# Optimization experiments

Hardware: AMD Instinct MI355X
Metric: run time of the kernel (lower is better)

Reference implementation:

```python
import jax, jax.numpy as jnp
import numpy as np

B, TV, TE = 128, 32, 64
VOCAB, EMB, H, REPR, NET, MAXLEN = 1024, 256, 512, 128, 8, 32


def setup_inputs() -> dict:
    key = jax.random.key(0)
    ks = jax.random.split(key, 26)
    g = lambda i, shape: jax.random.normal(ks[i], shape, dtype=jnp.float32) * 0.05
    return dict(
        input_vertex=jax.random.randint(ks[0], (B, TV), 0, VOCAB),
        input_edge=jax.random.randint(ks[1], (B, TE, 3), 0, NET),
        vertex_emb=g(2, (VOCAB, EMB)),
        v_Wi=g(3, (3 * H, EMB)), v_Wh=g(4, (3 * H, H)), v_bi=g(5, (3 * H,)), v_bh=g(6, (3 * H,)),
        vout_W=g(7, (VOCAB, H)), vout_b=g(8, (VOCAB,)),
        vrep_W=g(9, (REPR, H)), vrep_b=g(10, (REPR,)),
        edge_emb=g(11, (MAXLEN, EMB)),
        e_Wi=g(12, (3 * H, 2 * EMB)), e_Wh=g(13, (3 * H, H)), e_bi=g(14, (3 * H,)), e_bh=g(15, (3 * H,)),
        erep_W=g(16, (REPR, H)), erep_b=g(17, (REPR,)),
        etype_W=g(18, (NET, REPR)), etype_b=g(19, (NET,)),
        src_w=g(20, (REPR,)), src_b=g(21, ()),
        dst_w=g(22, (REPR,)), dst_b=g(23, ()),
    )


def _gru_scan(X, Wi, Wh, bi, bh):
    # X: [T, B, D] -> hidden states [T, B, H]; torch GRUCell gate order r,z,n
    gi = jnp.einsum('tbd,gd->tbg', X, Wi) + bi  # precompute input projections
    h0 = jnp.zeros((X.shape[1], Wh.shape[1]), X.dtype)

    def step(h, gi_t):
        gh = h @ Wh.T + bh
        ir, iz, inn = jnp.split(gi_t, 3, axis=-1)
        hr, hz, hn = jnp.split(gh, 3, axis=-1)
        r = jax.nn.sigmoid(ir + hr)
        z = jax.nn.sigmoid(iz + hz)
        n = jnp.tanh(inn + r * hn)
        h_new = (1.0 - z) * n + z * h
        return h_new, h_new

    _, hs = jax.lax.scan(step, h0, gi)
    return hs


def reference(input_vertex, input_edge, vertex_emb, v_Wi, v_Wh, v_bi, v_bh,
              vout_W, vout_b, vrep_W, vrep_b, edge_emb, e_Wi, e_Wh, e_bi, e_bh,
              erep_W, erep_b, etype_W, etype_b, src_w, src_b, dst_w, dst_b):
    # ---- vertex RNN ----
    Ve = vertex_emb[input_vertex].transpose(1, 0, 2)          # [Tv, B, emb]
    hv = _gru_scan(Ve, v_Wi, v_Wh, v_bi, v_bh)                # [Tv, B, H]
    O_vertex = jnp.einsum('tbh,vh->bvt', hv, vout_W) + vout_b[None, :, None]  # [B, vocab, Tv]
    vrep = jnp.einsum('tbh,rh->tbr', hv, vrep_W) + vrep_b     # [Tv, B, repr]

    # ---- edge RNN ----
    E = jnp.concatenate([edge_emb[input_edge[:, :, 0]],
                         edge_emb[input_edge[:, :, 1]]], axis=2)  # [B, Te, 2*emb]
    he = _gru_scan(E.transpose(1, 0, 2), e_Wi, e_Wh, e_bi, e_bh)  # [Te, B, H]
    e = jnp.einsum('tbh,rh->tbr', he, erep_W) + erep_b            # [Te, B, repr]
    O_edge_type = jnp.einsum('ebr,kr->bke', e, etype_W) + etype_b[None, :, None]  # [B, n_et, Te]

    # ---- edge-vertex additive attention: tanh(e + v) ----
    u = jnp.tanh(e[:, None] + vrep[None])                     # [Te, Tv, B, repr]
    osrc = jnp.einsum('evbr,r->bve', u, src_w) + src_b        # [B, Tv, Te]
    odst = jnp.einsum('evbr,r->bve', u, dst_w) + dst_b        # [B, Tv, Te]
    O_edge = jnp.stack([osrc, odst], axis=2)                  # [B, Tv, 2, Te]

    return O_vertex, O_edge, O_edge_type
```

## Files before the change

### kernel.cpp

```cpp
#include <hip/hip_runtime.h>
#include <hip/hip_bf16.h>


typedef __bf16 bf16_t;
typedef bf16_t bf16x8 __attribute__((ext_vector_type(8)));
typedef bf16_t bf16x4 __attribute__((ext_vector_type(4)));
typedef float  f32x4  __attribute__((ext_vector_type(4)));
typedef unsigned long long ull_t;

#define OFF_GIV  0ull
#define OFF_GIE  6291456ull
#define OFF_HV   18874368ull
#define OFF_HE   20971520ull
#define OFF_VREP 25165824ull
#define OFF_EREP 25690112ull
#define OFF_HBUF 26738688ull
#define FLAG_BYTE_OFF  54001664ull
#define GICNT_BYTE_OFF 54002176ull
#define OFF_CVT  27002880ull
#define CVT_VEMB  0ull
#define CVT_EEMB  262144ull
#define CVT_VWI   270336ull
#define CVT_EWI   663552ull
#define CVT_VWH   1449984ull
#define CVT_EWH   2236416ull
#define CVT_VOUT  3022848ull
#define CVT_VREPW 3547136ull
#define CVT_EREPW 3612672ull

#define OUT_OV 0ull
#define OUT_OE 4194304ull
#define OUT_OT 4718592ull

__device__ __forceinline__ float fsigmoid(float x) {
    float e = __builtin_amdgcn_exp2f(-x * 1.4426950408889634f);
    return __builtin_amdgcn_rcpf(1.0f + e);
}
__device__ __forceinline__ float ftanh(float x) {
    x = fminf(x, 15.0f);
    float e = __builtin_amdgcn_exp2f(x * 2.8853900817779268f);
    return (e - 1.0f) * __builtin_amdgcn_rcpf(e + 1.0f);
}

__global__ __launch_bounds__(256) void prep_kernel(
    const float* __restrict__ vemb, const float* __restrict__ eemb,
    const float* __restrict__ vwi,  const float* __restrict__ ewi,
    const float* __restrict__ vwh,  const float* __restrict__ ewh,
    const float* __restrict__ voutw, const float* __restrict__ vrepw,
    const float* __restrict__ erepw, bf16_t* __restrict__ cvt,
    int* __restrict__ gicnt)
{
    int blk = blockIdx.x;
    if (blk >= 3592) {
        if (threadIdx.x < 128) gicnt[threadIdx.x] = 0;
        return;
    }
    const float* src; bf16_t* dst; int lb;
    if (blk < 256)       { src = vemb;  dst = cvt + CVT_VEMB;  lb = blk; }
    else if (blk < 264)  { src = eemb;  dst = cvt + CVT_EEMB;  lb = blk - 256; }
    else if (blk < 648)  { src = vwi;   dst = cvt + CVT_VWI;   lb = blk - 264; }
    else if (blk < 1416) { src = ewi;   dst = cvt + CVT_EWI;   lb = blk - 648; }
    else if (blk < 2184) { src = vwh;   dst = cvt + CVT_VWH;   lb = blk - 1416; }
    else if (blk < 2952) { src = ewh;   dst = cvt + CVT_EWH;   lb = blk - 2184; }
    else if (blk < 3464) { src = voutw; dst = cvt + CVT_VOUT;  lb = blk - 2952; }
    else if (blk < 3528) { src = vrepw; dst = cvt + CVT_VREPW; lb = blk - 3464; }
    else                 { src = erepw; dst = cvt + CVT_EREPW; lb = blk - 3528; }
    int idx = lb * 1024 + threadIdx.x * 4;
    float4 v = *(const float4*)(src + idx);
    bf16x4 o;
    o[0] = (bf16_t)v.x; o[1] = (bf16_t)v.y; o[2] = (bf16_t)v.z; o[3] = (bf16_t)v.w;
    *(bf16x4*)(dst + idx) = o;
}

template<int GATHER, int K>
__device__ __forceinline__ void produce_gi(
    const bf16_t* __restrict__ W, const float* __restrict__ bias,
    bf16_t* __restrict__ C, const int* __restrict__ gidx,
    const bf16_t* __restrict__ emb, int* __restrict__ cnt, int bx, int nbase)
{
    constexpr int K32 = K / 32;
    const int tid = threadIdx.x, lane = tid & 63, wv = tid >> 6;
    const int r16 = lane & 15, quad = lane >> 4, koff = quad * 8;
    const int mbase = bx * 512 + wv * 64;

    const bf16_t* ap0[4];
    const bf16_t* ap1[4];
#pragma unroll
    for (int i = 0; i < 4; ++i) {
        int row = mbase + i * 16 + r16;
        int b = row & 127, t = row >> 7;
        if (GATHER == 1) {
            ap0[i] = emb + (size_t)gidx[b * 32 + t] * 256 + koff;
            ap1[i] = ap0[i];
        } else {
            int c = (b * 64 + t) * 3;
            ap0[i] = emb + (size_t)gidx[c] * 256 + koff;
            ap1[i] = emb + (size_t)gidx[c + 1] * 256 + koff;
        }
    }
    const bf16_t* bp[4];
#pragma unroll
    for (int j = 0; j < 4; ++j)
        bp[j] = W + (size_t)(nbase + j * 16 + r16) * K + koff;

    f32x4 acc[4][4];
#pragma unroll
    for (int i = 0; i < 4; ++i)
#pragma unroll
        for (int j = 0; j < 4; ++j) acc[i][j] = (f32x4){0.f, 0.f, 0.f, 0.f};

    for (int kc = 0; kc < K32; ++kc) {
        bf16x8 a[4], b[4];
#pragma unroll
        for (int i = 0; i < 4; ++i) {
            const bf16_t* p;
            if (GATHER == 2) p = (kc < 8) ? (ap0[i] + kc * 32) : (ap1[i] + (kc - 8) * 32);
            else             p = ap0[i] + kc * 32;
            a[i] = *(const bf16x8*)p;
        }
#pragma unroll
        for (int j = 0; j < 4; ++j) b[j] = *(const bf16x8*)(bp[j] + kc * 32);
#pragma unroll
        for (int i = 0; i < 4; ++i)
#pragma unroll
            for (int j = 0; j < 4; ++j)
                acc[i][j] = __builtin_amdgcn_mfma_f32_16x16x32_bf16(a[i], b[j], acc[i][j], 0, 0, 0);
    }

#pragma unroll
    for (int j = 0; j < 4; ++j) {
        int col = nbase + j * 16 + r16;
        float bf = bias[col];
#pragma unroll
        for (int i = 0; i < 4; ++i) {
#pragma unroll
            for (int q = 0; q < 4; ++q) {
                int row = mbase + i * 16 + quad * 4 + q;
                bf16_t hb = (bf16_t)(acc[i][j][q] + bf);
                __hip_atomic_store((unsigned short*)(C + (size_t)row * 1536 + col),
                                   __builtin_bit_cast(unsigned short, hb),
                                   __ATOMIC_RELAXED, __HIP_MEMORY_SCOPE_AGENT);
            }
        }
    }
    __builtin_amdgcn_s_waitcnt(0);
    __syncthreads();
    if (tid < 4)
        __hip_atomic_fetch_add(&cnt[bx * 4 + tid], 1,
                               __ATOMIC_RELAXED, __HIP_MEMORY_SCOPE_AGENT);
}

template<int OUTMODE, int K>
__device__ __forceinline__ void consume_gemm(
    const bf16_t* __restrict__ A, const bf16_t* __restrict__ W,
    const float* __restrict__ bias, void* __restrict__ Cv,
    int N, int bx, int nbase)
{
    constexpr int K32 = K / 32;
    const int tid = threadIdx.x, lane = tid & 63, wv = tid >> 6;
    const int r16 = lane & 15, quad = lane >> 4, koff = quad * 8;
    const int mbase = bx * 512 + wv * 64;

    const bf16_t* ap[4];
#pragma unroll
    for (int i = 0; i < 4; ++i)
        ap[i] = A + (size_t)(mbase + i * 16 + r16) * K + koff;
    const bf16_t* bp[4];
#pragma unroll
    for (int j = 0; j < 4; ++j)
        bp[j] = W + (size_t)(nbase + j * 16 + r16) * K + koff;

    f32x4 acc[4][4];
#pragma unroll
    for (int i = 0; i < 4; ++i)
#pragma unroll
        for (int j = 0; j < 4; ++j) acc[i][j] = (f32x4){0.f, 0.f, 0.f, 0.f};

    for (int kc = 0; kc < K32; ++kc) {
        bf16x8 a[4], b[4];
#pragma unroll
        for (int i = 0; i < 4; ++i) a[i] = *(const bf16x8*)(ap[i] + kc * 32);
#pragma unroll
        for (int j = 0; j < 4; ++j) b[j] = *(const bf16x8*)(bp[j] + kc * 32);
#pragma unroll
        for (int i = 0; i < 4; ++i)
#pragma unroll
            for (int j = 0; j < 4; ++j)
                acc[i][j] = __builtin_amdgcn_mfma_f32_16x16x32_bf16(a[i], b[j], acc[i][j], 0, 0, 0);
    }

#pragma unroll
    for (int j = 0; j < 4; ++j) {
        int col = nbase + j * 16 + r16;
        float bf = bias[col];
#pragma unroll
        for (int i = 0; i < 4; ++i) {
            int rowq = mbase + i * 16 + quad * 4;
            if (OUTMODE == 1) {
                int b = rowq >> 5, t0 = rowq & 31;
                float4 v4;
                v4.x = acc[i][j][0] + bf; v4.y = acc[i][j][1] + bf;
                v4.z = acc[i][j][2] + bf; v4.w = acc[i][j][3] + bf;
                *(float4*)((float*)Cv + ((size_t)(b * 1024) + col) * 32 + t0) = v4;
            } else {
                bf16_t* C = (bf16_t*)Cv;
#pragma unroll
                for (int q = 0; q < 4; ++q) {
                    bf16_t hb = (bf16_t)(acc[i][j][q] + bf);
                    __hip_atomic_store(
                        (unsigned short*)(C + (size_t)(rowq + q) * N + col),
                        __builtin_bit_cast(unsigned short, hb),
                        __ATOMIC_RELAXED, __HIP_MEMORY_SCOPE_AGENT);
                }
            }
        }
    }
}

__device__ __forceinline__ void gate_on(int* p, int thresh) {
    if (threadIdx.x == 0) {
        while (__hip_atomic_load(p, __ATOMIC_RELAXED,
                                 __HIP_MEMORY_SCOPE_AGENT) < thresh)
            __builtin_amdgcn_s_sleep(8);
    }
    __syncthreads();
    asm volatile("" ::: "memory");
}

__global__ __launch_bounds__(512) void fused_scan(
    bf16_t* __restrict__ giV, bf16_t* __restrict__ giE,
    const bf16_t* __restrict__ WhV, const bf16_t* __restrict__ WhE,
    const float* __restrict__ bhV, const float* __restrict__ bhE,
    bf16_t* __restrict__ hV, bf16_t* __restrict__ hE,
    bf16_t* __restrict__ hbuf, int* __restrict__ flags, int* __restrict__ gicnt,
    const int* __restrict__ ivtx, const int* __restrict__ iedg,
    const bf16_t* __restrict__ vemb, const bf16_t* __restrict__ eemb,
    const bf16_t* __restrict__ vwi, const bf16_t* __restrict__ ewi,
    const float* __restrict__ vbi, const float* __restrict__ ebi,
    const bf16_t* __restrict__ voutw, const float* __restrict__ voutb,
    const bf16_t* __restrict__ vrepw, const float* __restrict__ vrepb,
    const bf16_t* __restrict__ erepw, const float* __restrict__ erepb,
    bf16_t* __restrict__ vrep, bf16_t* __restrict__ erep,
    const float* __restrict__ etypeW, const float* __restrict__ etypeB,
    const float* __restrict__ src_w, const float* __restrict__ src_b,
    const float* __restrict__ dst_w, const float* __restrict__ dst_b,
    float* __restrict__ out)
{
    __shared__ __align__(16) char lds_all[83968];
    bf16_t (*hbf)[520] = (bf16_t (*)[520])lds_all;
    f32x4 (*red)[3][64] = (f32x4 (*)[3][64])(lds_all + 33280);

    const int bid = blockIdx.x;

    if (bid >= 128) {
        const int tid = threadIdx.x;
        if (bid < 512) {
            int g3 = bid - 128;
            int bx = g3 / 24, nb = g3 - bx * 24;
            produce_gi<2, 512>(ewi, ebi, giE, iedg, eemb, gicnt + 32, bx, nb * 64);
        } else if (bid < 704) {
            int g2 = bid - 512;
            int bx = g2 / 24, nb = g2 - bx * 24;
            produce_gi<1, 256>(vwi, vbi, giV, ivtx, vemb, gicnt, bx, nb * 64);
        } else if (bid < 832) {
            gate_on(&gicnt[96], 64);
            int cb = bid - 704;
            consume_gemm<1, 512>(hV, voutw, voutb, out, 1024, cb & 7, (cb >> 3) * 64);
        } else if (bid < 848) {
            gate_on(&gicnt[96], 64);
            int cb = bid - 832;
            consume_gemm<0, 512>(hV, vrepw, vrepb, vrep, 128, cb & 7, (cb >> 3) * 64);
            __builtin_amdgcn_s_waitcnt(0);
            __syncthreads();
            if (tid == 0)
                __hip_atomic_fetch_add(&gicnt[98], 1,
                                       __ATOMIC_RELAXED, __HIP_MEMORY_SCOPE_AGENT);
        } else if (bid < 880) {
            gate_on(&gicnt[97], 64);
            int cb = bid - 848;
            consume_gemm<0, 512>(hE, erepw, erepb, erep, 128, cb & 15, (cb >> 4) * 64);
            __builtin_amdgcn_s_waitcnt(0);
            __syncthreads();
            if (tid == 0)
                __hip_atomic_fetch_add(&gicnt[99], 1,
                                       __ATOMIC_RELAXED, __HIP_MEMORY_SCOPE_AGENT);
        } else if (bid < 1008) {
            gate_on(&gicnt[99], 32);
            int o = (bid - 880) * 512 + tid;
            int te = o & 63, k = (o >> 6) & 7, b = o >> 9;
            float sacc = etypeB[k];
            const bf16_t* e = erep + ((size_t)(b * 64 + te)) * 128;
            const float* wk = etypeW + k * 128;
#pragma unroll 8
            for (int r = 0; r < 128; ++r) sacc += (float)e[r] * wk[r];
            out[OUT_OT + o] = sacc;
        } else {
            gate_on(&gicnt[99], 32);
            gate_on(&gicnt[98], 16);
            float (*es)[129] = (float (*)[129])lds_all;
            float (*vs)[129] = (float (*)[129])(lds_all + 33024);
            float* swf = (float*)(lds_all + 49536);
            float* dwf = (float*)(lds_all + 50048);
            int b = bid - 1008;
            for (int f = tid; f < 64 * 128; f += 512) {
                int i = f >> 7, r = f & 127;
                es[i][r] = (float)erep[((size_t)(b * 64 + i)) * 128 + r];
            }
            for (int f = tid; f < 32 * 128; f += 512) {
                int i = f >> 7, r = f & 127;
                vs[i][r] = (float)vrep[((size_t)(b * 32 + i)) * 128 + r];
            }
            if (tid < 128) { swf[tid] = src_w[tid]; dwf[tid] = dst_w[tid]; }
            __syncthreads();
            float sb = src_b[0], db = dst_b[0];
            for (int p = tid; p < 2048; p += 512) {
                int te = p & 63, tv = p >> 6;
                float sacc = 0.f, dacc = 0.f;
#pragma unroll 4
                for (int r = 0; r < 128; ++r) {
                    float u = ftanh(es[te][r] + vs[tv][r]);
                    sacc += u * swf[r];
                    dacc += u * dwf[r];
                }
                size_t base = OUT_OE + ((size_t)(b * 32 + tv) * 2) * 64;
                out[base + te]      = sacc + sb;
                out[base + 64 + te] = dacc + db;
            }
        }
        return;
    }

    const int role = bid >> 6;
    const int lb   = bid & 63;
    const int g    = lb & 7;
    const int s    = lb >> 3;
    const bf16_t* gi = role ? giE : giV;
    const bf16_t* Wh = role ? WhE : WhV;
    const float*  bh = role ? bhE : bhV;
    bf16_t* hout = role ? hE : hV;
    const int T = role ? 64 : 32;
    const int slot = role * 8 + g;
    bf16_t* buf0 = hbuf + (size_t)slot * 16384;
    int* fl = flags + slot * 8;
    int* gc = role ? (gicnt + 32) : gicnt;
    int* done = role ? &gicnt[97] : &gicnt[96];
    const int bb = g * 16;

    const int tid = threadIdx.x, lane = tid & 63, w = tid >> 6;
    const int team = w >> 1, half = w & 1;
    const int r16 = lane & 15, quad = lane >> 4, koff = quad * 8;
    const int j = s * 64 + team * 16 + r16;
    const int kbase = half * 256;

    bf16x8 wfrag[3][8];
#pragma unroll
    for (int gate = 0; gate < 3; ++gate) {
        const bf16_t* wrow = Wh + ((size_t)(gate * 512 + j)) * 512 + kbase + koff;
#pragma unroll
        for (int kc = 0; kc < 8; ++kc)
            wfrag[gate][kc] = *(const bf16x8*)(wrow + kc * 32);
    }
    const float bhr = bh[j], bhz = bh[512 + j], bhn = bh[1024 + j];
    float hq[4] = {0.f, 0.f, 0.f, 0.f};

    for (int u = tid; u < 16 * 520; u += 512)
        ((bf16_t*)hbf)[u] = (bf16_t)0.f;
    __syncthreads();

    for (int t = 0; t < T; ++t) {
        if (w == 0) {
            while (__hip_atomic_load(&gc[t], __ATOMIC_RELAXED,
                                     __HIP_MEMORY_SCOPE_AGENT) < 24)
                __builtin_amdgcn_s_sleep(2);
        }
        __syncthreads();
        asm volatile("" ::: "memory");

        float gv[3][4];
        if (half == 0) {
#pragma unroll
            for (int gg = 0; gg < 3; ++gg)
#pragma unroll
                for (int q = 0; q < 4; ++q)
                    gv[gg][q] = (float)gi[((size_t)(t * 128 + bb + quad * 4 + q)) * 1536
                                          + gg * 512 + j];
        }

        if (t > 0) {
            if (w == 1) {
                while (!__all((int)(__hip_atomic_load(&fl[lane & 7], __ATOMIC_RELAXED,
                                                      __HIP_MEMORY_SCOPE_AGENT) >= t))) { }
            }
            __syncthreads();
            asm volatile("" ::: "memory");
            ull_t* src = (ull_t*)(buf0 + (size_t)(t & 1) * 8192);
#pragma unroll
            for (int k = 0; k < 4; ++k) {
                int u = tid + k * 512;
                ull_t vv = __hip_atomic_load(src + u, __ATOMIC_RELAXED,
                                             __HIP_MEMORY_SCOPE_AGENT);
                *(ull_t*)&hbf[u >> 7][(u & 127) * 4] = vv;
            }
        }
        __syncthreads();

        f32x4 ar = {0.f,0.f,0.f,0.f}, az = {0.f,0.f,0.f,0.f}, an = {0.f,0.f,0.f,0.f};
#pragma unroll
        for (int kc = 0; kc < 8; ++kc) {
            bf16x8 a = *(const bf16x8*)&hbf[r16][kbase + kc * 32 + koff];
            ar = __builtin_amdgcn_mfma_f32_16x16x32_bf16(a, wfrag[0][kc], ar, 0, 0, 0);
            az = __builtin_amdgcn_mfma_f32_16x16x32_bf16(a, wfrag[1][kc], az, 0, 0, 0);
            an = __builtin_amdgcn_mfma_f32_16x16x32_bf16(a, wfrag[2][kc], an, 0, 0, 0);
        }

        if (half == 1) {
            red[team][0][lane] = ar;
            red[team][1][lane] = az;
            red[team][2][lane] = an;
        }
        __syncthreads();

        bf16_t hb4[4];
        if (half == 0) {
            ar += red[team][0][lane];
            az += red[team][1][lane];
            an += red[team][2][lane];
#pragma unroll
            for (int q = 0; q < 4; ++q) {
                float r = fsigmoid(gv[0][q] + ar[q] + bhr);
                float z = fsigmoid(gv[1][q] + az[q] + bhz);
                float n = ftanh(gv[2][q] + r * (an[q] + bhn));
                float hnew = (1.0f - z) * n + z * hq[q];
                hq[q] = hnew;
                hb4[q] = (bf16_t)hnew;
            }
            if (t + 1 < T) {
                bf16_t* dstg = buf0 + (size_t)((t + 1) & 1) * 8192;
#pragma unroll
                for (int q = 0; q < 4; ++q)
                    __hip_atomic_store(
                        (unsigned short*)(dstg + (quad * 4 + q) * 512 + j),
                        __builtin_bit_cast(unsigned short, hb4[q]),
                        __ATOMIC_RELAXED, __HIP_MEMORY_SCOPE_AGENT);
            }
        }

        if (t + 1 < T) {
            __builtin_amdgcn_s_waitcnt(0);
            __syncthreads();
            if (tid == 0)
                __hip_atomic_store(&fl[s], t + 1,
                                   __ATOMIC_RELAXED, __HIP_MEMORY_SCOPE_AGENT);
        } else {
            __syncthreads();
        }
        if (half == 0) {
#pragma unroll
            for (int q = 0; q < 4; ++q)
                __hip_atomic_store(
                    (unsigned short*)(hout + ((size_t)((bb + quad * 4 + q) * T + t)) * 512 + j),
                    __builtin_bit_cast(unsigned short, hb4[q]),
                    __ATOMIC_RELAXED, __HIP_MEMORY_SCOPE_AGENT);
        }
    }

    __builtin_amdgcn_s_waitcnt(0);
    __syncthreads();
    if (tid == 0)
        __hip_atomic_fetch_add(done, 1, __ATOMIC_RELAXED, __HIP_MEMORY_SCOPE_AGENT);
}

extern "C" void kernel_launch(void* const* d_in, const int* in_sizes, int n_in,
                              void* d_out, int out_size, void* d_ws, size_t ws_size,
                              hipStream_t stream)
{
    const int*   input_vertex = (const int*)d_in[0];
    const int*   input_edge   = (const int*)d_in[1];
    const float* vertex_emb   = (const float*)d_in[2];
    const float* v_Wi  = (const float*)d_in[3];
    const float* v_Wh  = (const float*)d_in[4];
    const float* v_bi  = (const float*)d_in[5];
    const float* v_bh  = (const float*)d_in[6];
    const float* vout_W = (const float*)d_in[7];
    const float* vout_b = (const float*)d_in[8];
    const float* vrep_W = (const float*)d_in[9];
    const float* vrep_b = (const float*)d_in[10];
    const float* edge_emb = (const float*)d_in[11];
    const float* e_Wi  = (const float*)d_in[12];
    const float* e_Wh  = (const float*)d_in[13];
    const float* e_bi  = (const float*)d_in[14];
    const float* e_bh  = (const float*)d_in[15];
    const float* erep_W = (const float*)d_in[16];
    const float* erep_b = (const float*)d_in[17];
    const float* etype_W = (const float*)d_in[18];
    const float* etype_b = (const float*)d_in[19];
    const float* src_w = (const float*)d_in[20];
    const float* src_b = (const float*)d_in[21];
    const float* dst_w = (const float*)d_in[22];
    const float* dst_b = (const float*)d_in[23];

    bf16_t* ws   = (bf16_t*)d_ws;
    bf16_t* giV  = ws + OFF_GIV;
    bf16_t* giE  = ws + OFF_GIE;
    bf16_t* hV   = ws + OFF_HV;
    bf16_t* hE   = ws + OFF_HE;
    bf16_t* vrep = ws + OFF_VREP;
    bf16_t* erep = ws + OFF_EREP;
    bf16_t* hbuf = ws + OFF_HBUF;
    bf16_t* cvt  = ws + OFF_CVT;
    int*    flags = (int*)((char*)d_ws + FLAG_BYTE_OFF);
    int*    gicnt = (int*)((char*)d_ws + GICNT_BYTE_OFF);
    float*  out  = (float*)d_out;

    prep_kernel<<<3593, 256, 0, stream>>>(vertex_emb, edge_emb, v_Wi, e_Wi, v_Wh, e_Wh,
                                          vout_W, vrep_W, erep_W, cvt, gicnt);

    fused_scan<<<1136, 512, 0, stream>>>(
        giV, giE, cvt + CVT_VWH, cvt + CVT_EWH, v_bh, e_bh, hV, hE,
        hbuf, flags, gicnt, input_vertex, input_edge,
        cvt + CVT_VEMB, cvt + CVT_EEMB, cvt + CVT_VWI, cvt + CVT_EWI,
        v_bi, e_bi,
        cvt + CVT_VOUT, vout_b, cvt + CVT_VREPW, vrep_b,
        cvt + CVT_EREPW, erep_b, vrep, erep,
        etype_W, etype_b, src_w, src_b, dst_w, dst_b, out);
}
```

Baseline: 434.9 us.

## Fold weight bf16 conversion into fused kernel with grid-wide gate

Removes the separate prep kernel and has the first 256 blocks of the fused kernel convert fp32 weights/embeddings to bf16, then signal a global counter that the other early blocks wait on. Counter initialization moves to a memset. This removes a kernel launch and the serialization between kernels. In exchange it relies on all converter blocks being co-resident and adds a spin barrier before the scan and GI producers can start.

```diff
diff --git a/kernel.cpp b/kernel.cpp
--- a/kernel.cpp
+++ b/kernel.cpp
@@ -42,36 +42,6 @@
     return (e - 1.0f) * __builtin_amdgcn_rcpf(e + 1.0f);
 }
 
-__global__ __launch_bounds__(256) void prep_kernel(
-    const float* __restrict__ vemb, const float* __restrict__ eemb,
-    const float* __restrict__ vwi,  const float* __restrict__ ewi,
-    const float* __restrict__ vwh,  const float* __restrict__ ewh,
-    const float* __restrict__ voutw, const float* __restrict__ vrepw,
-    const float* __restrict__ erepw, bf16_t* __restrict__ cvt,
-    int* __restrict__ gicnt)
-{
-    int blk = blockIdx.x;
-    if (blk >= 3592) {
-        if (threadIdx.x < 128) gicnt[threadIdx.x] = 0;
-        return;
-    }
-    const float* src; bf16_t* dst; int lb;
-    if (blk < 256)       { src = vemb;  dst = cvt + CVT_VEMB;  lb = blk; }
-    else if (blk < 264)  { src = eemb;  dst = cvt + CVT_EEMB;  lb = blk - 256; }
-    else if (blk < 648)  { src = vwi;   dst = cvt + CVT_VWI;   lb = blk - 264; }
-    else if (blk < 1416) { src = ewi;   dst = cvt + CVT_EWI;   lb = blk - 648; }
-    else if (blk < 2184) { src = vwh;   dst = cvt + CVT_VWH;   lb = blk - 1416; }
-    else if (blk < 2952) { src = ewh;   dst = cvt + CVT_EWH;   lb = blk - 2184; }
-    else if (blk < 3464) { src = voutw; dst = cvt + CVT_VOUT;  lb = blk - 2952; }
-    else if (blk < 3528) { src = vrepw; dst = cvt + CVT_VREPW; lb = blk - 3464; }
-    else                 { src = erepw; dst = cvt + CVT_EREPW; lb = blk - 3528; }
-    int idx = lb * 1024 + threadIdx.x * 4;
-    float4 v = *(const float4*)(src + idx);
-    bf16x4 o;
-    o[0] = (bf16_t)v.x; o[1] = (bf16_t)v.y; o[2] = (bf16_t)v.z; o[3] = (bf16_t)v.w;
-    *(bf16x4*)(dst + idx) = o;
-}
-
 template<int GATHER, int K>
 __device__ __forceinline__ void produce_gi(
     const bf16_t* __restrict__ W, const float* __restrict__ bias,
@@ -244,6 +214,11 @@
     const float* __restrict__ etypeW, const float* __restrict__ etypeB,
     const float* __restrict__ src_w, const float* __restrict__ src_b,
     const float* __restrict__ dst_w, const float* __restrict__ dst_b,
+    const float* __restrict__ f_vemb, const float* __restrict__ f_eemb,
+    const float* __restrict__ f_vwi,  const float* __restrict__ f_ewi,
+    const float* __restrict__ f_vwh,  const float* __restrict__ f_ewh,
+    const float* __restrict__ f_voutw, const float* __restrict__ f_vrepw,
+    const float* __restrict__ f_erepw, bf16_t* __restrict__ cvt,
     float* __restrict__ out)
 {
     __shared__ __align__(16) char lds_all[83968];
@@ -251,6 +226,38 @@
     f32x4 (*red)[3][64] = (f32x4 (*)[3][64])(lds_all + 33280);
 
     const int bid = blockIdx.x;
+
+    if (bid < 256) {
+        const int tid = threadIdx.x;
+        for (int k = 0; k < 15; ++k) {
+            int blk = bid * 15 + k;
+            if (blk >= 3592) break;
+            const float* src; bf16_t* dst; int lb;
+            if (blk < 256)       { src = f_vemb;  dst = cvt + CVT_VEMB;  lb = blk; }
+            else if (blk < 264)  { src = f_eemb;  dst = cvt + CVT_EEMB;  lb = blk - 256; }
+            else if (blk < 648)  { src = f_vwi;   dst = cvt + CVT_VWI;   lb = blk - 264; }
+            else if (blk < 1416) { src = f_ewi;   dst = cvt + CVT_EWI;   lb = blk - 648; }
+            else if (blk < 2184) { src = f_vwh;   dst = cvt + CVT_VWH;   lb = blk - 1416; }
+            else if (blk < 2952) { src = f_ewh;   dst = cvt + CVT_EWH;   lb = blk - 2184; }
+            else if (blk < 3464) { src = f_voutw; dst = cvt + CVT_VOUT;  lb = blk - 2952; }
+            else if (blk < 3528) { src = f_vrepw; dst = cvt + CVT_VREPW; lb = blk - 3464; }
+            else                 { src = f_erepw; dst = cvt + CVT_EREPW; lb = blk - 3528; }
+            int idx = lb * 1024 + tid * 2;
+            float2 v = *(const float2*)(src + idx);
+            unsigned int pk =
+                (unsigned int)__builtin_bit_cast(unsigned short, (bf16_t)v.x) |
+                ((unsigned int)__builtin_bit_cast(unsigned short, (bf16_t)v.y) << 16);
+            __hip_atomic_store((unsigned int*)(dst + idx), pk,
+                               __ATOMIC_RELAXED, __HIP_MEMORY_SCOPE_AGENT);
+        }
+        __builtin_amdgcn_s_waitcnt(0);
+        __syncthreads();
+        if (tid == 0)
+            __hip_atomic_fetch_add(&gicnt[100], 1,
+                                   __ATOMIC_RELAXED, __HIP_MEMORY_SCOPE_AGENT);
+    }
+    if (bid < 704)
+        gate_on(&gicnt[100], 256);
 
     if (bid >= 128) {
         const int tid = threadIdx.x;
@@ -512,8 +519,7 @@
     int*    gicnt = (int*)((char*)d_ws + GICNT_BYTE_OFF);
     float*  out  = (float*)d_out;
 
-    prep_kernel<<<3593, 256, 0, stream>>>(vertex_emb, edge_emb, v_Wi, e_Wi, v_Wh, e_Wh,
-                                          vout_W, vrep_W, erep_W, cvt, gicnt);
+    hipMemsetAsync((char*)d_ws + FLAG_BYTE_OFF, 0, 1024, stream);
 
     fused_scan<<<1136, 512, 0, stream>>>(
         giV, giE, cvt + CVT_VWH, cvt + CVT_EWH, v_bh, e_bh, hV, hE,
@@ -522,5 +528,7 @@
         v_bi, e_bi,
         cvt + CVT_VOUT, vout_b, cvt + CVT_VREPW, vrep_b,
         cvt + CVT_EREPW, erep_b, vrep, erep,
-        etype_W, etype_b, src_w, src_b, dst_w, dst_b, out);
-}
+        etype_W, etype_b, src_w, src_b, dst_w, dst_b,
+        vertex_emb, edge_emb, v_Wi, e_Wi, v_Wh, e_Wh,
+        vout_W, vrep_W, erep_W, cvt, out);
+}
```

Result: slower. 445.4 us (+2.4%).
